# Performance work log

Measured on AMD Instinct MI355X. Metric: run time of the kernel, lower is better.

## Reference

```python
import jax, jax.numpy as jnp
import numpy as np

DIM = 256
RADIUS = 3
DIAM = 2 * RADIUS + 1          # 7
NNEIGH = DIAM * DIAM           # 49
B, H, W = 2, 64, 64
EPS_LN = 1e-6
EPS_NORM = 1e-7


def conv1x1(x, w, b):
    # x: [B,Cin,H,W], w: [Cout,Cin], b: [Cout]
    return jnp.einsum('oi,bihw->bohw', w, x) + b[None, :, None, None]


def layernorm2d(x, g, b):
    # channel-wise norm as in LayerNorm2d (mean/var over channel dim)
    u = x.mean(1, keepdims=True)
    s = ((x - u) ** 2).mean(1, keepdims=True)
    xn = (x - u) / jnp.sqrt(s + EPS_LN)
    return g[None, :, None, None] * xn + b[None, :, None, None]


def unfold_reflect(x, r):
    # torch F.unfold(pad(x, reflect, r), kernel=2r+1).reshape(B,C,D*D,H,W)
    d = 2 * r + 1
    hh, ww = x.shape[2], x.shape[3]
    xp = jnp.pad(x, ((0, 0), (0, 0), (r, r), (r, r)), mode='reflect')
    pats = [xp[:, :, i:i + hh, j:j + ww] for i in range(d) for j in range(d)]
    return jnp.stack(pats, axis=2)  # [B,C,D*D,H,W]


def setup_inputs() -> dict:
    key = jax.random.key(0)
    ks = jax.random.split(key, 20)
    sc_c = 1.0 / np.sqrt(DIM)
    sc_f = 1.0 / np.sqrt(NNEIGH + DIM)
    inp = {
        'spatial_feats': jax.random.normal(ks[0], (B, DIM, H, W), jnp.float32),
        'semantic_feats': jax.random.normal(ks[1], (B, DIM, H, W), jnp.float32),
        # range_proj: conv1x1 -> LN2d -> SiLU -> conv1x1
        'rp_w1': jax.random.normal(ks[2], (DIM, DIM), jnp.float32) * sc_c,
        'rp_b1': jnp.zeros((DIM,), jnp.float32),
        'rp_g': jnp.ones((DIM,), jnp.float32),
        'rp_be': jnp.zeros((DIM,), jnp.float32),
        'rp_w2': jax.random.normal(ks[3], (DIM, DIM), jnp.float32) * sc_c,
        'rp_b2': jnp.zeros((DIM,), jnp.float32),
        # fixup_proj: conv1x1(49+C->49) -> LN2d -> SiLU -> conv1x1(49->49)
        'fp_w1': jax.random.normal(ks[4], (NNEIGH, NNEIGH + DIM), jnp.float32) * sc_f,
        'fp_b1': jnp.zeros((NNEIGH,), jnp.float32),
        'fp_g': jnp.ones((NNEIGH,), jnp.float32),
        'fp_be': jnp.zeros((NNEIGH,), jnp.float32),
        'fp_w2': jax.random.normal(ks[5], (NNEIGH, NNEIGH), jnp.float32) * (1.0 / np.sqrt(NNEIGH)),
        'fp_b2': jnp.zeros((NNEIGH,), jnp.float32),
        # output_proj: conv1x1 -> LN2d -> conv1x1
        'op_w1': jax.random.normal(ks[6], (DIM, DIM), jnp.float32) * sc_c,
        'op_b1': jnp.zeros((DIM,), jnp.float32),
        'op_g': jnp.ones((DIM,), jnp.float32),
        'op_be': jnp.zeros((DIM,), jnp.float32),
        'op_w2': jax.random.normal(ks[7], (DIM, DIM), jnp.float32) * sc_c,
        'op_b2': jnp.zeros((DIM,), jnp.float32),
        'sigma_spatial': jnp.ones((), jnp.float32),
    }
    return inp


def reference(spatial_feats, semantic_feats,
              rp_w1, rp_b1, rp_g, rp_be, rp_w2, rp_b2,
              fp_w1, fp_b1, fp_g, fp_be, fp_w2, fp_b2,
              op_w1, op_b1, op_g, op_be, op_w2, op_b2,
              sigma_spatial):
    scale = jnp.asarray(DIM ** 0.5, spatial_feats.dtype)
    # range_proj(semantic_feats)
    px = conv1x1(semantic_feats, rp_w1, rp_b1)
    px = jax.nn.silu(layernorm2d(px, rp_g, rp_be))
    px = conv1x1(px, rp_w2, rp_b2)  # [B,C,H,W]

    # spatial (Gaussian) kernel over the window
    lin = jnp.linspace(-1.0, 1.0, DIAM)
    xg, yg = jnp.meshgrid(lin, lin, indexing='ij')
    spatial_kernel = jnp.exp(-(xg ** 2 + yg ** 2) / (2.0 * sigma_spatial ** 2))
    spatial_kernel = spatial_kernel.reshape(1, NNEIGH, 1, 1)

    # range kernel: local similarity + softmax over the 49 neighbors
    queries = unfold_reflect(px, RADIUS)                       # [B,C,N,H,W]
    sim = jnp.einsum('bcnhw,bchw->bnhw', queries, px) / scale
    range_kernel = jax.nn.softmax(sim.astype(jnp.float32), axis=1).astype(px.dtype)

    # neighborhoods of spatial features
    neighborhoods = unfold_reflect(spatial_feats, RADIUS)      # [B,C,N,H,W]

    # gated fixup correction
    ck = range_kernel * spatial_kernel                          # [B,N,H,W]
    fx = conv1x1(jnp.concatenate([ck, semantic_feats], axis=1), fp_w1, fp_b1)
    fx = jax.nn.silu(layernorm2d(fx, fp_g, fp_be))
    fx = conv1x1(fx, fp_w2, fp_b2)
    ck = ck + ck * jax.nn.sigmoid(fx)
    ck = ck / (ck.sum(1, keepdims=True) + EPS_NORM)

    # weighted neighborhood sum
    out = jnp.einsum('bcnhw,bnhw->bchw', neighborhoods, ck)

    # output_proj (note: no SiLU here, matching the module)
    out = conv1x1(out, op_w1, op_b1)
    out = layernorm2d(out, op_g, op_be)
    out = conv1x1(out, op_w2, op_b2)
    return out
```

## Files before the change

### kernel.cpp

```cpp
#include <hip/hip_runtime.h>
#include <cstdint>

#define HW 4096
#define C_ 256
#define NN 49
#define KW 305

typedef __bf16 bf16;
typedef bf16 bf16x8 __attribute__((ext_vector_type(8)));
typedef bf16 bf16x4 __attribute__((ext_vector_type(4)));
typedef bf16 bf16x2 __attribute__((ext_vector_type(2)));
typedef float f32x4 __attribute__((ext_vector_type(4)));

#define GLD16(src, dst) __builtin_amdgcn_global_load_lds( \
    (const __attribute__((address_space(1))) uint32_t*)(src), \
    (__attribute__((address_space(3))) uint32_t*)(dst), 16, 0, 0)

__device__ __forceinline__ int refl(int i) { return i < 0 ? -i : (i > 63 ? 126 - i : i); }
__device__ __forceinline__ float sigmoidf_(float x) { return 1.f / (1.f + __expf(-x)); }

__global__ __launch_bounds__(256) void prep_all(const float* __restrict__ rp_w1,
                                                const float* __restrict__ rp_w2,
                                                const float* __restrict__ op_w1,
                                                const float* __restrict__ op_w2,
                                                const float* __restrict__ fp_w1,
                                                const float* __restrict__ sigma,
                                                bf16* __restrict__ wrp1, bf16* __restrict__ wrp2,
                                                bf16* __restrict__ wop1, bf16* __restrict__ wop2,
                                                float* __restrict__ w1ckg, bf16* __restrict__ w1sb,
                                                float* __restrict__ sk)
{
    int bid = blockIdx.x;
    if (bid < 256) {
        const float* src = (bid < 64) ? rp_w1 : (bid < 128) ? rp_w2 : (bid < 192) ? op_w1 : op_w2;
        bf16* dst = (bid < 64) ? wrp1 : (bid < 128) ? wrp2 : (bid < 192) ? wop1 : wop2;
        int i = ((bid & 63) * 256 + threadIdx.x) * 4;
        f32x4 v = *(const f32x4*)&src[i];
        bf16x4 o = {(bf16)v[0], (bf16)v[1], (bf16)v[2], (bf16)v[3]};
        *(bf16x4*)&dst[i] = o;
    } else if (bid == 256) {
        int n = threadIdx.x;
        if (n < NN) {
            int i = n / 7, j = n % 7;
            float xg = (i - 3) * (1.f / 3.f), yg = (j - 3) * (1.f / 3.f);
            float s = sigma[0];
            sk[n] = __expf(-(xg * xg + yg * yg) / (2.f * s * s));
        }
    } else if (bid < 270) {
        int idx = (bid - 257) * 256 + threadIdx.x;
        if (idx < NN * 64) {
            int k = idx >> 6, o = idx & 63;
            w1ckg[idx] = (o < NN) ? fp_w1[o * KW + k] : 0.f;
        }
    } else {
        int idx = (bid - 270) * 256 + threadIdx.x;
        int o = idx >> 8, c = idx & 255;
        w1sb[idx] = (o < NN) ? (bf16)fp_w1[o * KW + NN + c] : (bf16)0.f;
    }
}

__global__ __launch_bounds__(256) void cvtT_k(const float* __restrict__ spatial,
                                              const float* __restrict__ semantic,
                                              bf16* __restrict__ spb, bf16* __restrict__ seb)
{
    __shared__ float tile[32][33];
    int z = blockIdx.z;
    int b = z & 1;
    const float* src = (z >> 1) ? semantic : spatial;
    bf16* dst = (z >> 1) ? seb : spb;
    int p0 = blockIdx.x * 32, c0 = blockIdx.y * 32;
    int tx = threadIdx.x & 31, ty = threadIdx.x >> 5;
    const float* s = src + (size_t)b * C_ * HW;
    #pragma unroll
    for (int i = 0; i < 32; i += 8)
        tile[ty + i][tx] = s[(size_t)(c0 + ty + i) * HW + p0 + tx];
    __syncthreads();
    int p = threadIdx.x >> 3, cq = (threadIdx.x & 7) * 4;
    bf16x4 o = {(bf16)tile[cq][p], (bf16)tile[cq + 1][p], (bf16)tile[cq + 2][p], (bf16)tile[cq + 3][p]};
    *(bf16x4*)&dst[((size_t)b * HW + p0 + p) * C_ + c0 + cq] = o;
}

__device__ __forceinline__ void stage_b(const bf16* __restrict__ Wp, bf16* dst, int kc, int t)
{
    const bf16* gB = Wp + (size_t)(t >> 2) * C_ + kc + (((t & 3) ^ ((t >> 3) & 3)) * 8);
    #pragma unroll
    for (int ii = 0; ii < 4; ++ii)
        GLD16(gB + (size_t)ii * 64 * C_, dst + ii * 2048 + t * 8);
}

template<bool SILU, int MODE>
__global__ __launch_bounds__(256) void conv_pair(const bf16* __restrict__ X,
                                                 const bf16* __restrict__ W1,
                                                 const float* __restrict__ b1v,
                                                 const float* __restrict__ g,
                                                 const float* __restrict__ be,
                                                 const bf16* __restrict__ W2,
                                                 const float* __restrict__ b2v,
                                                 void* __restrict__ Yv)
{
    __shared__ bf16 Xf[16 * 256];
    __shared__ bf16 Mid[16 * 256];
    __shared__ bf16 Bs[2][256 * 32];
    __shared__ float lnred[16][4][2];
    const int t = threadIdx.x;
    const int lane = t & 63, wc = t >> 6;
    const int l15 = lane & 15, kb = lane >> 4;
    const long q0 = (long)blockIdx.x * 16;

    {
        const int row = t >> 5, slot = t & 31;
        const bf16* gX = X + (q0 + row) * C_ + (slot ^ (row & 7)) * 8;
        GLD16(gX, &Xf[t * 8]);
        GLD16(gX + 8 * C_, &Xf[2048 + t * 8]);
    }
    stage_b(W1, &Bs[0][0], 0, t);

    const int ax7 = l15 & 7;
    const int bsl = (kb ^ ((l15 >> 1) & 3)) * 8;
    int boff[4];
    #pragma unroll
    for (int n = 0; n < 4; ++n)
        boff[n] = (wc * 64 + n * 16 + l15) * 32 + bsl;

    f32x4 acc[4];
    #pragma unroll
    for (int n = 0; n < 4; ++n) acc[n] = (f32x4){0.f, 0.f, 0.f, 0.f};

    __syncthreads();
    int cur = 0;
    #pragma unroll
    for (int ks = 0; ks < 8; ++ks) {
        if (ks < 7) stage_b(W1, &Bs[cur ^ 1][0], (ks + 1) * 32, t);
        bf16x8 a = *(const bf16x8*)&Xf[l15 * 256 + ((ks * 4 + kb) ^ ax7) * 8];
        #pragma unroll
        for (int n = 0; n < 4; ++n) {
            bf16x8 b = *(const bf16x8*)&Bs[cur][boff[n]];
            acc[n] = __builtin_amdgcn_mfma_f32_16x16x32_bf16(a, b, acc[n], 0, 0, 0);
        }
        __syncthreads();
        cur ^= 1;
    }

    stage_b(W2, &Bs[0][0], 0, t);

    float s4[4] = {0.f, 0.f, 0.f, 0.f}, ss4[4] = {0.f, 0.f, 0.f, 0.f};
    #pragma unroll
    for (int n = 0; n < 4; ++n) {
        float bo = b1v[wc * 64 + n * 16 + l15];
        #pragma unroll
        for (int r = 0; r < 4; ++r) {
            float v = acc[n][r] + bo;
            acc[n][r] = v;
            s4[r] += v; ss4[r] += v * v;
        }
    }
    #pragma unroll
    for (int off = 1; off <= 8; off <<= 1) {
        #pragma unroll
        for (int r = 0; r < 4; ++r) {
            s4[r]  += __shfl_xor(s4[r], off, 64);
            ss4[r] += __shfl_xor(ss4[r], off, 64);
        }
    }
    if (l15 == 0) {
        #pragma unroll
        for (int r = 0; r < 4; ++r) {
            lnred[kb * 4 + r][wc][0] = s4[r];
            lnred[kb * 4 + r][wc][1] = ss4[r];
        }
    }
    __syncthreads();
    float mean[4], rstd[4];
    #pragma unroll
    for (int r = 0; r < 4; ++r) {
        int p = kb * 4 + r;
        float st  = lnred[p][0][0] + lnred[p][1][0] + lnred[p][2][0] + lnred[p][3][0];
        float sst = lnred[p][0][1] + lnred[p][1][1] + lnred[p][2][1] + lnred[p][3][1];
        mean[r] = st * (1.f / 256.f);
        float var = sst * (1.f / 256.f) - mean[r] * mean[r];
        rstd[r] = rsqrtf(var + 1e-6f);
    }
    #pragma unroll
    for (int n = 0; n < 4; ++n) {
        int ch = wc * 64 + n * 16 + l15;
        float gv = g[ch], bev = be[ch];
        #pragma unroll
        for (int r = 0; r < 4; ++r) {
            float y = (acc[n][r] - mean[r]) * rstd[r] * gv + bev;
            if (SILU) y *= sigmoidf_(y);
            int p = kb * 4 + r;
            Mid[p * 256 + (((ch >> 3) ^ (p & 7)) * 8) + (ch & 7)] = (bf16)y;
        }
    }
    __syncthreads();

    f32x4 acc2[4];
    #pragma unroll
    for (int n = 0; n < 4; ++n) acc2[n] = (f32x4){0.f, 0.f, 0.f, 0.f};
    cur = 0;
    #pragma unroll
    for (int ks = 0; ks < 8; ++ks) {
        if (ks < 7) stage_b(W2, &Bs[cur ^ 1][0], (ks + 1) * 32, t);
        bf16x8 a = *(const bf16x8*)&Mid[l15 * 256 + ((ks * 4 + kb) ^ ax7) * 8];
        #pragma unroll
        for (int n = 0; n < 4; ++n) {
            bf16x8 b = *(const bf16x8*)&Bs[cur][boff[n]];
            acc2[n] = __builtin_amdgcn_mfma_f32_16x16x32_bf16(a, b, acc2[n], 0, 0, 0);
        }
        __syncthreads();
        cur ^= 1;
    }

    if constexpr (MODE == 0) {
        #pragma unroll
        for (int n = 0; n < 4; ++n) {
            int ch = wc * 64 + n * 16 + l15;
            float bo = b2v[ch];
            #pragma unroll
            for (int r = 0; r < 4; ++r)
                Xf[(kb * 4 + r) * 256 + ch] = (bf16)(acc2[n][r] + bo);
        }
        __syncthreads();
        bf16* Y = (bf16*)Yv;
        const int p = t >> 4, cb = (t & 15) * 16;
        bf16x8 v0 = *(const bf16x8*)&Xf[p * 256 + cb];
        bf16x8 v1 = *(const bf16x8*)&Xf[p * 256 + cb + 8];
        *(bf16x8*)&Y[(q0 + p) * C_ + cb] = v0;
        *(bf16x8*)&Y[(q0 + p) * C_ + cb + 8] = v1;
    } else {
        float* Y = (float*)Yv;
        const int bb = (int)(q0 >> 12);
        const int pp = (int)(q0 & 4095) + kb * 4;
        #pragma unroll
        for (int n = 0; n < 4; ++n) {
            int ch = wc * 64 + n * 16 + l15;
            float bo = b2v[ch];
            f32x4 val = {acc2[n][0] + bo, acc2[n][1] + bo, acc2[n][2] + bo, acc2[n][3] + bo};
            *(f32x4*)&Y[((size_t)bb * C_ + ch) * HW + pp] = val;
        }
    }
}

__global__ __launch_bounds__(256) void attn_k(const bf16* __restrict__ px,
                                              const bf16* __restrict__ spb,
                                              const bf16* __restrict__ seb,
                                              const bf16* __restrict__ w1sb,
                                              const float* __restrict__ w1ckg,
                                              const float* __restrict__ b1,
                                              const float* __restrict__ w2,
                                              const float* __restrict__ b2,
                                              const float* __restrict__ g,
                                              const float* __restrict__ be,
                                              const float* __restrict__ sk,
                                              bf16* __restrict__ outb)
{
    __shared__ float S[112 * 17];
    __shared__ float fxs[64 * 17];
    __shared__ float w1ck[NN * 64];
    __shared__ float w2l[NN][51];
    __shared__ float ckl[16][64];
    __shared__ float hb[4][64];
    __shared__ bf16 spatl[128 * 128];

    const int t = threadIdx.x, lane = t & 63, wid = t >> 6;
    const int l15 = lane & 15, kb = lane >> 4;
    const int blk = blockIdx.x;
    const int batch = blk >> 8, tt = blk & 255;
    const int h0 = (tt >> 4) * 4, w0 = (tt & 15) * 4;
    const long base = (long)batch * HW;

    #pragma unroll
    for (int i = 0; i < 13; ++i) {
        int idx = i * 256 + t;
        if (idx < NN * 64) w1ck[idx] = w1ckg[idx];
    }
    for (int idx = t; idx < NN * NN; idx += 256)
        w2l[idx / NN][idx % NN] = w2[idx];

    const int ppy = l15 >> 2, ppx = l15 & 3;
    const long qB = base + (h0 + ppy) * 64 + (w0 + ppx);
    const bf16* bpxp = px + qB * C_ + kb * 8;
    const bf16* bsemp = seb + qB * C_ + kb * 8;

    bool valid[3], ispx[3];
    const bf16* arow[3];
    #pragma unroll
    for (int j = 0; j < 3; ++j) {
        int tid = wid + 4 * j;
        valid[j] = tid < 11;
        ispx[j] = tid < 7;
        int u = tid * 16 + l15;
        int uy = (u * 205) >> 11, ux = u - uy * 10;
        long grow = (u < 100) ? base + refl(h0 + uy - 3) * 64 + refl(w0 + ux - 3) : base;
        int o = (tid - 7) * 16 + l15;
        arow[j] = ispx[j] ? (px + grow * C_ + kb * 8)
                          : (w1sb + (size_t)(o & 63) * C_ + kb * 8);
    }

    f32x4 acc[3];
    #pragma unroll
    for (int j = 0; j < 3; ++j) acc[j] = (f32x4){0.f, 0.f, 0.f, 0.f};

    #pragma unroll
    for (int ks = 0; ks < 8; ++ks) {
        bf16x8 bp = *(const bf16x8*)(bpxp + ks * 32);
        bf16x8 bs = *(const bf16x8*)(bsemp + ks * 32);
        #pragma unroll
        for (int j = 0; j < 3; ++j) {
            if (valid[j]) {
                bf16x8 a = *(const bf16x8*)(arow[j] + ks * 32);
                acc[j] = __builtin_amdgcn_mfma_f32_16x16x32_bf16(a, ispx[j] ? bp : bs, acc[j], 0, 0, 0);
            }
        }
    }
    #pragma unroll
    for (int j = 0; j < 3; ++j) {
        if (valid[j]) {
            int tid = wid + 4 * j;
            float* dst = ispx[j] ? &S[(tid * 16 + kb * 4) * 17 + l15]
                                 : &fxs[((tid - 7) * 16 + kb * 4) * 17 + l15];
            dst[0] = acc[j][0]; dst[17] = acc[j][1]; dst[34] = acc[j][2]; dst[51] = acc[j][3];
        }
    }

    const bf16* growp[8];
    {
        const int us = t >> 4, ss = t & 15;
        #pragma unroll
        for (int i = 0; i < 8; ++i) {
            int uu = i * 16 + us;
            int uy = (uu * 205) >> 11, ux = uu - uy * 10;
            long grow = (uu < 100) ? base + refl(h0 + uy - 3) * 64 + refl(w0 + ux - 3) : base;
            growp[i] = spb + grow * C_ + ss * 8;
            GLD16(growp[i], &spatl[uu * 128 + ss * 8]);
        }
    }
    __syncthreads();

    const float skv = (lane < NN) ? sk[lane] : 0.f;
    const int nn_ = (lane < NN) ? lane : 0;
    const int dy = nn_ / 7, dx = nn_ % 7;
    #pragma unroll
    for (int j = 0; j < 4; ++j) {
        int p = wid * 4 + j, py = p >> 2, px4 = p & 3;
        int u = (py + dy) * 10 + px4 + dx;
        float sval = (lane < NN) ? S[u * 17 + p] * 0.0625f : -1e30f;
        float mx = sval;
        #pragma unroll
        for (int off = 32; off; off >>= 1) mx = fmaxf(mx, __shfl_xor(mx, off, 64));
        float ev = (lane < NN) ? __expf(sval - mx) : 0.f;
        float ssum = ev;
        #pragma unroll
        for (int off = 32; off; off >>= 1) ssum += __shfl_xor(ssum, off, 64);
        ckl[p][lane] = (lane < NN) ? (ev / ssum) * skv : 0.f;
    }

    const float bo  = (lane < NN) ? b1[lane] : 0.f;
    const float gl  = (lane < NN) ? g[lane] : 0.f;
    const float bel = (lane < NN) ? be[lane] : 0.f;
    const float b2l = (lane < NN) ? b2[lane] : 0.f;
    #pragma unroll
    for (int j = 0; j < 4; ++j) {
        int p = wid * 4 + j;
        float fx = fxs[lane * 17 + p] + bo;
        #pragma unroll 7
        for (int k = 0; k < NN; ++k) fx += w1ck[k * 64 + lane] * ckl[p][k];
        float s = fx, ss = fx * fx;
        #pragma unroll
        for (int off = 32; off; off >>= 1) {
            s  += __shfl_xor(s, off, 64);
            ss += __shfl_xor(ss, off, 64);
        }
        float mean = s * (1.f / 49.f);
        float var  = ss * (1.f / 49.f) - mean * mean;
        float rstd = rsqrtf(var + 1e-6f);
        float hv = 0.f;
        if (lane < NN) {
            float xn = (fx - mean) * rstd * gl + bel;
            hv = xn * sigmoidf_(xn);
        }
        hb[wid][lane] = hv;
        float ckv = 0.f;
        if (lane < NN) {
            float fx2 = b2l;
            #pragma unroll 7
            for (int k = 0; k < NN; ++k) fx2 += w2l[lane][k] * hb[wid][k];
            ckv = ckl[p][lane] * (1.f + sigmoidf_(fx2));
        }
        float tot = ckv;
        #pragma unroll
        for (int off = 32; off; off >>= 1) tot += __shfl_xor(tot, off, 64);
        ckl[p][lane] = (lane < NN) ? ckv / (tot + 1e-7f) : 0.f;
    }

    #pragma unroll
    for (int ci = 0; ci < 2; ++ci) {
        if (ci == 1) {
            __syncthreads();
            const int ss = t & 15;
            #pragma unroll
            for (int i = 0; i < 8; ++i) {
                int uu = i * 16 + (t >> 4);
                GLD16(growp[i] + 128, &spatl[uu * 128 + ss * 8]);
            }
            __syncthreads();
        }
        #pragma unroll
        for (int j = 0; j < 4; ++j) {
            int p = wid * 4 + j, py = p >> 2, px4 = p & 3;
            long q = base + (h0 + py) * 64 + (w0 + px4);
            int ub = py * 10 + px4;
            float a0 = 0.f, a1 = 0.f;
            #pragma unroll
            for (int n = 0; n < NN; ++n) {
                int u = ub + (n / 7) * 10 + (n % 7);
                float cv = ckl[p][n];
                bf16x2 v = *(const bf16x2*)&spatl[u * 128 + lane * 2];
                a0 += cv * (float)v[0];
                a1 += cv * (float)v[1];
            }
            bf16x2 ov = {(bf16)a0, (bf16)a1};
            *(bf16x2*)&outb[q * C_ + ci * 128 + lane * 2] = ov;
        }
    }
}

extern "C" void kernel_launch(void* const* d_in, const int* in_sizes, int n_in,
                              void* d_out, int out_size, void* d_ws, size_t ws_size,
                              hipStream_t stream)
{
    const float* spatial  = (const float*)d_in[0];
    const float* semantic = (const float*)d_in[1];
    const float* rp_w1 = (const float*)d_in[2];
    const float* rp_b1 = (const float*)d_in[3];
    const float* rp_g  = (const float*)d_in[4];
    const float* rp_be = (const float*)d_in[5];
    const float* rp_w2 = (const float*)d_in[6];
    const float* rp_b2 = (const float*)d_in[7];
    const float* fp_w1 = (const float*)d_in[8];
    const float* fp_b1 = (const float*)d_in[9];
    const float* fp_g  = (const float*)d_in[10];
    const float* fp_be = (const float*)d_in[11];
    const float* fp_w2 = (const float*)d_in[12];
    const float* fp_b2 = (const float*)d_in[13];
    const float* op_w1 = (const float*)d_in[14];
    const float* op_b1 = (const float*)d_in[15];
    const float* op_g  = (const float*)d_in[16];
    const float* op_be = (const float*)d_in[17];
    const float* op_w2 = (const float*)d_in[18];
    const float* op_b2 = (const float*)d_in[19];
    const float* sigma = (const float*)d_in[20];

    const size_t NPX = 2 * (size_t)HW;
    float* ws = (float*)d_ws;
    float* sk    = ws;
    float* w1ckg = sk + 64;
    bf16* bfbase = (bf16*)(w1ckg + 3200);
    bf16* spb = bfbase;
    bf16* seb = spb + NPX * C_;
    bf16* t0  = seb + NPX * C_;
    bf16* t1  = t0  + NPX * C_;
    bf16* wrp1 = t1 + NPX * C_;
    bf16* wrp2 = wrp1 + C_ * C_;
    bf16* wop1 = wrp2 + C_ * C_;
    bf16* wop2 = wop1 + C_ * C_;
    bf16* w1sb = wop2 + C_ * C_;

    prep_all<<<334, 256, 0, stream>>>(rp_w1, rp_w2, op_w1, op_w2, fp_w1, sigma,
                                      wrp1, wrp2, wop1, wop2, w1ckg, w1sb, sk);
    cvtT_k<<<dim3(128, 8, 4), 256, 0, stream>>>(spatial, semantic, spb, seb);

    conv_pair<true, 0><<<512, 256, 0, stream>>>(seb, wrp1, rp_b1, rp_g, rp_be, wrp2, rp_b2, t1);

    attn_k<<<512, 256, 0, stream>>>(t1, spb, seb, w1sb, w1ckg, fp_b1, fp_w2, fp_b2,
                                    fp_g, fp_be, sk, t0);

    conv_pair<false, 1><<<512, 256, 0, stream>>>(t0, wop1, op_b1, op_g, op_be, wop2, op_b2, d_out);
}
```

Baseline: 75.54 us.

## Merge prep kernels, double conv row tile, restructure attention staging

Fuses the weight-prep and transpose kernels into one setup launch, and doubles the conv_pair tile to 32 pixels so each staged weight tile feeds two MFMA row groups, halving the grid. The attention kernel now stages the full 256-channel spatial neighborhood once into a swizzled shared buffer, where the old code made two 128-channel passes. The similarity MFMAs reuse that shared buffer, the fixup weights are held in registers or stored as bf16 transposed, and the weighted sum uses 8-wide vector loads. This trims launch overhead, global reloads and barriers, but conv_pair runs fewer blocks and attention needs more registers and shared memory, which can lower occupancy.

```diff
diff --git a/kernel.cpp b/kernel.cpp
--- a/kernel.cpp
+++ b/kernel.cpp
@@ -19,65 +19,72 @@
 __device__ __forceinline__ int refl(int i) { return i < 0 ? -i : (i > 63 ? 126 - i : i); }
 __device__ __forceinline__ float sigmoidf_(float x) { return 1.f / (1.f + __expf(-x)); }
 
-__global__ __launch_bounds__(256) void prep_all(const float* __restrict__ rp_w1,
-                                                const float* __restrict__ rp_w2,
-                                                const float* __restrict__ op_w1,
-                                                const float* __restrict__ op_w2,
-                                                const float* __restrict__ fp_w1,
-                                                const float* __restrict__ sigma,
-                                                bf16* __restrict__ wrp1, bf16* __restrict__ wrp2,
-                                                bf16* __restrict__ wop1, bf16* __restrict__ wop2,
-                                                float* __restrict__ w1ckg, bf16* __restrict__ w1sb,
-                                                float* __restrict__ sk)
+__global__ __launch_bounds__(256) void setup_k(const float* __restrict__ spatial,
+                                               const float* __restrict__ semantic,
+                                               const float* __restrict__ rp_w1,
+                                               const float* __restrict__ rp_w2,
+                                               const float* __restrict__ op_w1,
+                                               const float* __restrict__ op_w2,
+                                               const float* __restrict__ fp_w1,
+                                               const float* __restrict__ fp_w2,
+                                               const float* __restrict__ sigma,
+                                               bf16* __restrict__ spb, bf16* __restrict__ seb,
+                                               bf16* __restrict__ wrp1, bf16* __restrict__ wrp2,
+                                               bf16* __restrict__ wop1, bf16* __restrict__ wop2,
+                                               float* __restrict__ w1ckg, bf16* __restrict__ w1sb,
+                                               bf16* __restrict__ w2Tg, float* __restrict__ sk)
 {
-    int bid = blockIdx.x;
-    if (bid < 256) {
-        const float* src = (bid < 64) ? rp_w1 : (bid < 128) ? rp_w2 : (bid < 192) ? op_w1 : op_w2;
-        bf16* dst = (bid < 64) ? wrp1 : (bid < 128) ? wrp2 : (bid < 192) ? wop1 : wop2;
-        int i = ((bid & 63) * 256 + threadIdx.x) * 4;
+    __shared__ float tile[32][33];
+    const int bid = blockIdx.x, t = threadIdx.x;
+    if (bid < 4096) {
+        int z = bid >> 10, r = bid & 1023;
+        int b = z & 1;
+        const float* src = (z >> 1) ? semantic : spatial;
+        bf16* dst = (z >> 1) ? seb : spb;
+        int p0 = (r & 127) * 32, c0 = (r >> 7) * 32;
+        int tx = t & 31, ty = t >> 5;
+        const float* s = src + (size_t)b * C_ * HW;
+        #pragma unroll
+        for (int i = 0; i < 32; i += 8)
+            tile[ty + i][tx] = s[(size_t)(c0 + ty + i) * HW + p0 + tx];
+        __syncthreads();
+        int p = t >> 3, cq = (t & 7) * 4;
+        bf16x4 o = {(bf16)tile[cq][p], (bf16)tile[cq + 1][p], (bf16)tile[cq + 2][p], (bf16)tile[cq + 3][p]};
+        *(bf16x4*)&dst[((size_t)b * HW + p0 + p) * C_ + c0 + cq] = o;
+        return;
+    }
+    int pid = bid - 4096;
+    if (pid < 256) {
+        const float* src = (pid < 64) ? rp_w1 : (pid < 128) ? rp_w2 : (pid < 192) ? op_w1 : op_w2;
+        bf16* dst = (pid < 64) ? wrp1 : (pid < 128) ? wrp2 : (pid < 192) ? wop1 : wop2;
+        int i = ((pid & 63) * 256 + t) * 4;
         f32x4 v = *(const f32x4*)&src[i];
         bf16x4 o = {(bf16)v[0], (bf16)v[1], (bf16)v[2], (bf16)v[3]};
         *(bf16x4*)&dst[i] = o;
-    } else if (bid == 256) {
-        int n = threadIdx.x;
-        if (n < NN) {
-            int i = n / 7, j = n % 7;
+    } else if (pid == 256) {
+        if (t < NN) {
+            int i = t / 7, j = t % 7;
             float xg = (i - 3) * (1.f / 3.f), yg = (j - 3) * (1.f / 3.f);
             float s = sigma[0];
-            sk[n] = __expf(-(xg * xg + yg * yg) / (2.f * s * s));
-        }
-    } else if (bid < 270) {
-        int idx = (bid - 257) * 256 + threadIdx.x;
+            sk[t] = __expf(-(xg * xg + yg * yg) / (2.f * s * s));
+        }
+    } else if (pid < 270) {
+        int idx = (pid - 257) * 256 + t;
         if (idx < NN * 64) {
             int k = idx >> 6, o = idx & 63;
             w1ckg[idx] = (o < NN) ? fp_w1[o * KW + k] : 0.f;
         }
-    } else {
-        int idx = (bid - 270) * 256 + threadIdx.x;
+    } else if (pid < 334) {
+        int idx = (pid - 270) * 256 + t;
         int o = idx >> 8, c = idx & 255;
         w1sb[idx] = (o < NN) ? (bf16)fp_w1[o * KW + NN + c] : (bf16)0.f;
-    }
-}
-
-__global__ __launch_bounds__(256) void cvtT_k(const float* __restrict__ spatial,
-                                              const float* __restrict__ semantic,
-                                              bf16* __restrict__ spb, bf16* __restrict__ seb)
-{
-    __shared__ float tile[32][33];
-    int z = blockIdx.z;
-    int b = z & 1;
-    const float* src = (z >> 1) ? semantic : spatial;
-    bf16* dst = (z >> 1) ? seb : spb;
-    int p0 = blockIdx.x * 32, c0 = blockIdx.y * 32;
-    int tx = threadIdx.x & 31, ty = threadIdx.x >> 5;
-    const float* s = src + (size_t)b * C_ * HW;
-    #pragma unroll
-    for (int i = 0; i < 32; i += 8)
-        tile[ty + i][tx] = s[(size_t)(c0 + ty + i) * HW + p0 + tx];
-    __syncthreads();
-    int p = threadIdx.x >> 3, cq = (threadIdx.x & 7) * 4;
-    bf16x4 o = {(bf16)tile[cq][p], (bf16)tile[cq + 1][p], (bf16)tile[cq + 2][p], (bf16)tile[cq + 3][p]};
-    *(bf16x4*)&dst[((size_t)b * HW + p0 + p) * C_ + c0 + cq] = o;
+    } else {
+        int idx = (pid - 334) * 256 + t;
+        if (idx < NN * 64) {
+            int k = idx >> 6, o = idx & 63;
+            w2Tg[idx] = (o < NN) ? (bf16)fp_w2[o * NN + k] : (bf16)0.f;
+        }
+    }
 }
 
 __device__ __forceinline__ void stage_b(const bf16* __restrict__ Wp, bf16* dst, int kc, int t)
@@ -98,44 +105,52 @@
                                                  const float* __restrict__ b2v,
                                                  void* __restrict__ Yv)
 {
-    __shared__ bf16 Xf[16 * 256];
-    __shared__ bf16 Mid[16 * 256];
-    __shared__ bf16 Bs[2][256 * 32];
-    __shared__ float lnred[16][4][2];
+    __shared__ __align__(16) bf16 Xf[32 * 256];
+    __shared__ __align__(16) bf16 Mid[32 * 256];
+    __shared__ __align__(16) bf16 Bs[2][256 * 32];
+    __shared__ float lnred[32][4][2];
     const int t = threadIdx.x;
     const int lane = t & 63, wc = t >> 6;
     const int l15 = lane & 15, kb = lane >> 4;
-    const long q0 = (long)blockIdx.x * 16;
+    const long q0 = (long)blockIdx.x * 32;
 
     {
-        const int row = t >> 5, slot = t & 31;
-        const bf16* gX = X + (q0 + row) * C_ + (slot ^ (row & 7)) * 8;
-        GLD16(gX, &Xf[t * 8]);
-        GLD16(gX + 8 * C_, &Xf[2048 + t * 8]);
+        const int r8 = t >> 5, slot = t & 31;
+        const bf16* gX = X + (q0 + r8) * C_ + ((slot ^ (r8 & 7)) * 8);
+        #pragma unroll
+        for (int i = 0; i < 4; ++i)
+            GLD16(gX + (size_t)i * 8 * C_, &Xf[i * 2048 + t * 8]);
     }
     stage_b(W1, &Bs[0][0], 0, t);
 
-    const int ax7 = l15 & 7;
+    const int x7 = l15 & 7;
     const int bsl = (kb ^ ((l15 >> 1) & 3)) * 8;
     int boff[4];
     #pragma unroll
     for (int n = 0; n < 4; ++n)
         boff[n] = (wc * 64 + n * 16 + l15) * 32 + bsl;
-
-    f32x4 acc[4];
-    #pragma unroll
-    for (int n = 0; n < 4; ++n) acc[n] = (f32x4){0.f, 0.f, 0.f, 0.f};
+    const int a0base = l15 * 256;
+    const int a1base = (16 + l15) * 256;
+
+    f32x4 acc[2][4];
+    #pragma unroll
+    for (int m = 0; m < 2; ++m)
+        #pragma unroll
+        for (int n = 0; n < 4; ++n) acc[m][n] = (f32x4){0.f, 0.f, 0.f, 0.f};
 
     __syncthreads();
     int cur = 0;
     #pragma unroll
     for (int ks = 0; ks < 8; ++ks) {
         if (ks < 7) stage_b(W1, &Bs[cur ^ 1][0], (ks + 1) * 32, t);
-        bf16x8 a = *(const bf16x8*)&Xf[l15 * 256 + ((ks * 4 + kb) ^ ax7) * 8];
+        const int ko = ((ks * 4 + kb) ^ x7) * 8;
+        bf16x8 a0 = *(const bf16x8*)&Xf[a0base + ko];
+        bf16x8 a1 = *(const bf16x8*)&Xf[a1base + ko];
         #pragma unroll
         for (int n = 0; n < 4; ++n) {
             bf16x8 b = *(const bf16x8*)&Bs[cur][boff[n]];
-            acc[n] = __builtin_amdgcn_mfma_f32_16x16x32_bf16(a, b, acc[n], 0, 0, 0);
+            acc[0][n] = __builtin_amdgcn_mfma_f32_16x16x32_bf16(a0, b, acc[0][n], 0, 0, 0);
+            acc[1][n] = __builtin_amdgcn_mfma_f32_16x16x32_bf16(a1, b, acc[1][n], 0, 0, 0);
         }
         __syncthreads();
         cur ^= 1;
@@ -143,69 +158,87 @@
 
     stage_b(W2, &Bs[0][0], 0, t);
 
-    float s4[4] = {0.f, 0.f, 0.f, 0.f}, ss4[4] = {0.f, 0.f, 0.f, 0.f};
+    float s4[2][4], ss4[2][4];
+    #pragma unroll
+    for (int m = 0; m < 2; ++m)
+        #pragma unroll
+        for (int r = 0; r < 4; ++r) { s4[m][r] = 0.f; ss4[m][r] = 0.f; }
     #pragma unroll
     for (int n = 0; n < 4; ++n) {
         float bo = b1v[wc * 64 + n * 16 + l15];
         #pragma unroll
+        for (int m = 0; m < 2; ++m)
+            #pragma unroll
+            for (int r = 0; r < 4; ++r) {
+                float v = acc[m][n][r] + bo;
+                acc[m][n][r] = v;
+                s4[m][r] += v; ss4[m][r] += v * v;
+            }
+    }
+    #pragma unroll
+    for (int off = 1; off <= 8; off <<= 1)
+        #pragma unroll
+        for (int m = 0; m < 2; ++m)
+            #pragma unroll
+            for (int r = 0; r < 4; ++r) {
+                s4[m][r]  += __shfl_xor(s4[m][r], off, 64);
+                ss4[m][r] += __shfl_xor(ss4[m][r], off, 64);
+            }
+    if (l15 == 0) {
+        #pragma unroll
+        for (int m = 0; m < 2; ++m)
+            #pragma unroll
+            for (int r = 0; r < 4; ++r) {
+                lnred[m * 16 + kb * 4 + r][wc][0] = s4[m][r];
+                lnred[m * 16 + kb * 4 + r][wc][1] = ss4[m][r];
+            }
+    }
+    __syncthreads();
+    float mean[2][4], rstd[2][4];
+    #pragma unroll
+    for (int m = 0; m < 2; ++m)
+        #pragma unroll
         for (int r = 0; r < 4; ++r) {
-            float v = acc[n][r] + bo;
-            acc[n][r] = v;
-            s4[r] += v; ss4[r] += v * v;
-        }
-    }
-    #pragma unroll
-    for (int off = 1; off <= 8; off <<= 1) {
-        #pragma unroll
-        for (int r = 0; r < 4; ++r) {
-            s4[r]  += __shfl_xor(s4[r], off, 64);
-            ss4[r] += __shfl_xor(ss4[r], off, 64);
-        }
-    }
-    if (l15 == 0) {
-        #pragma unroll
-        for (int r = 0; r < 4; ++r) {
-            lnred[kb * 4 + r][wc][0] = s4[r];
-            lnred[kb * 4 + r][wc][1] = ss4[r];
-        }
-    }
-    __syncthreads();
-    float mean[4], rstd[4];
-    #pragma unroll
-    for (int r = 0; r < 4; ++r) {
-        int p = kb * 4 + r;
-        float st  = lnred[p][0][0] + lnred[p][1][0] + lnred[p][2][0] + lnred[p][3][0];
-        float sst = lnred[p][0][1] + lnred[p][1][1] + lnred[p][2][1] + lnred[p][3][1];
-        mean[r] = st * (1.f / 256.f);
-        float var = sst * (1.f / 256.f) - mean[r] * mean[r];
-        rstd[r] = rsqrtf(var + 1e-6f);
-    }
+            int p = m * 16 + kb * 4 + r;
+            float st  = lnred[p][0][0] + lnred[p][1][0] + lnred[p][2][0] + lnred[p][3][0];
+            float sst = lnred[p][0][1] + lnred[p][1][1] + lnred[p][2][1] + lnred[p][3][1];
+            mean[m][r] = st * (1.f / 256.f);
+            float var = sst * (1.f / 256.f) - mean[m][r] * mean[m][r];
+            rstd[m][r] = rsqrtf(var + 1e-6f);
+        }
     #pragma unroll
     for (int n = 0; n < 4; ++n) {
         int ch = wc * 64 + n * 16 + l15;
         float gv = g[ch], bev = be[ch];
         #pragma unroll
-        for (int r = 0; r < 4; ++r) {
-            float y = (acc[n][r] - mean[r]) * rstd[r] * gv + bev;
-            if (SILU) y *= sigmoidf_(y);
-            int p = kb * 4 + r;
-            Mid[p * 256 + (((ch >> 3) ^ (p & 7)) * 8) + (ch & 7)] = (bf16)y;
-        }
+        for (int m = 0; m < 2; ++m)
+            #pragma unroll
+            for (int r = 0; r < 4; ++r) {
+                float y = (acc[m][n][r] - mean[m][r]) * rstd[m][r] * gv + bev;
+                if (SILU) y *= sigmoidf_(y);
+                int p = m * 16 + kb * 4 + r;
+                Mid[p * 256 + (((ch >> 3) ^ (p & 7)) * 8) + (ch & 7)] = (bf16)y;
+            }
     }
     __syncthreads();
 
-    f32x4 acc2[4];
-    #pragma unroll
-    for (int n = 0; n < 4; ++n) acc2[n] = (f32x4){0.f, 0.f, 0.f, 0.f};
+    f32x4 acc2[2][4];
+    #pragma unroll
+    for (int m = 0; m < 2; ++m)
+        #pragma unroll
+        for (int n = 0; n < 4; ++n) acc2[m][n] = (f32x4){0.f, 0.f, 0.f, 0.f};
     cur = 0;
     #pragma unroll
     for (int ks = 0; ks < 8; ++ks) {
         if (ks < 7) stage_b(W2, &Bs[cur ^ 1][0], (ks + 1) * 32, t);
-        bf16x8 a = *(const bf16x8*)&Mid[l15 * 256 + ((ks * 4 + kb) ^ ax7) * 8];
+        const int ko = ((ks * 4 + kb) ^ x7) * 8;
+        bf16x8 a0 = *(const bf16x8*)&Mid[a0base + ko];
+        bf16x8 a1 = *(const bf16x8*)&Mid[a1base + ko];
         #pragma unroll
         for (int n = 0; n < 4; ++n) {
             bf16x8 b = *(const bf16x8*)&Bs[cur][boff[n]];
-            acc2[n] = __builtin_amdgcn_mfma_f32_16x16x32_bf16(a, b, acc2[n], 0, 0, 0);
+            acc2[0][n] = __builtin_amdgcn_mfma_f32_16x16x32_bf16(a0, b, acc2[0][n], 0, 0, 0);
+            acc2[1][n] = __builtin_amdgcn_mfma_f32_16x16x32_bf16(a1, b, acc2[1][n], 0, 0, 0);
         }
         __syncthreads();
         cur ^= 1;
@@ -217,26 +250,33 @@
             int ch = wc * 64 + n * 16 + l15;
             float bo = b2v[ch];
             #pragma unroll
-            for (int r = 0; r < 4; ++r)
-                Xf[(kb * 4 + r) * 256 + ch] = (bf16)(acc2[n][r] + bo);
+            for (int m = 0; m < 2; ++m)
+                #pragma unroll
+                for (int r = 0; r < 4; ++r)
+                    Xf[(m * 16 + kb * 4 + r) * 256 + ch] = (bf16)(acc2[m][n][r] + bo);
         }
         __syncthreads();
         bf16* Y = (bf16*)Yv;
-        const int p = t >> 4, cb = (t & 15) * 16;
-        bf16x8 v0 = *(const bf16x8*)&Xf[p * 256 + cb];
-        bf16x8 v1 = *(const bf16x8*)&Xf[p * 256 + cb + 8];
-        *(bf16x8*)&Y[(q0 + p) * C_ + cb] = v0;
-        *(bf16x8*)&Y[(q0 + p) * C_ + cb + 8] = v1;
+        const int p = t >> 3, cb = (t & 7) * 32;
+        #pragma unroll
+        for (int i = 0; i < 4; ++i) {
+            bf16x8 v = *(const bf16x8*)&Xf[p * 256 + cb + i * 8];
+            *(bf16x8*)&Y[(q0 + p) * C_ + cb + i * 8] = v;
+        }
     } else {
         float* Y = (float*)Yv;
         const int bb = (int)(q0 >> 12);
-        const int pp = (int)(q0 & 4095) + kb * 4;
         #pragma unroll
         for (int n = 0; n < 4; ++n) {
             int ch = wc * 64 + n * 16 + l15;
             float bo = b2v[ch];
-            f32x4 val = {acc2[n][0] + bo, acc2[n][1] + bo, acc2[n][2] + bo, acc2[n][3] + bo};
-            *(f32x4*)&Y[((size_t)bb * C_ + ch) * HW + pp] = val;
+            #pragma unroll
+            for (int m = 0; m < 2; ++m) {
+                int pp = (int)(q0 & 4095) + m * 16 + kb * 4;
+                f32x4 val = {acc2[m][n][0] + bo, acc2[m][n][1] + bo,
+                             acc2[m][n][2] + bo, acc2[m][n][3] + bo};
+                *(f32x4*)&Y[((size_t)bb * C_ + ch) * HW + pp] = val;
+            }
         }
     }
 }
@@ -246,21 +286,20 @@
                                               const bf16* __restrict__ seb,
                                               const bf16* __restrict__ w1sb,
                                               const float* __restrict__ w1ckg,
+                                              const bf16* __restrict__ w2Tg,
                                               const float* __restrict__ b1,
-                                              const float* __restrict__ w2,
                                               const float* __restrict__ b2,
                                               const float* __restrict__ g,
                                               const float* __restrict__ be,
                                               const float* __restrict__ sk,
                                               bf16* __restrict__ outb)
 {
+    __shared__ __align__(16) bf16 uni[112 * 256];
     __shared__ float S[112 * 17];
     __shared__ float fxs[64 * 17];
-    __shared__ float w1ck[NN * 64];
-    __shared__ float w2l[NN][51];
+    __shared__ __align__(16) bf16 w2lT[NN * 64];
     __shared__ float ckl[16][64];
     __shared__ float hb[4][64];
-    __shared__ bf16 spatl[128 * 128];
 
     const int t = threadIdx.x, lane = t & 63, wid = t >> 6;
     const int l15 = lane & 15, kb = lane >> 4;
@@ -269,73 +308,87 @@
     const int h0 = (tt >> 4) * 4, w0 = (tt & 15) * 4;
     const long base = (long)batch * HW;
 
+    {
+        #pragma unroll
+        for (int i = 0; i < 13; ++i) {
+            int st = i * 256 + t;
+            if (st < 3200) {
+                int u = st >> 5, s = st & 31;
+                int uy = (u * 205) >> 11, ux = u - uy * 10;
+                long grow = base + refl(h0 + uy - 3) * 64 + refl(w0 + ux - 3);
+                GLD16(px + grow * C_ + ((s ^ (u & 7)) * 8), &uni[u * 256 + s * 8]);
+            }
+        }
+        GLD16(w2Tg + t * 8, &w2lT[t * 8]);
+        if (t < 136) GLD16(w2Tg + (256 + t) * 8, &w2lT[(256 + t) * 8]);
+    }
+
+    const int ppy = l15 >> 2, ppx = l15 & 3;
+    const int u_p = 33 + ppy * 10 + ppx;
+    const int bpbase = u_p * 256, bx7 = u_p & 7;
+    const long qB = base + (h0 + ppy) * 64 + (w0 + ppx);
+    const bf16* bsemp = seb + qB * C_ + kb * 8;
+    const int x7 = l15 & 7;
+
+    const int tid0 = wid, tid1 = wid + 4, tid2 = wid + 8;
+    const bool t1sim = (tid1 < 7);
+    const bool t2valid = (tid2 < 11);
+    const int a0base = (tid0 * 16 + l15) * 256;
+    const int a1base = (tid1 * 16 + l15) * 256;
+    const bf16* a1g = w1sb + (size_t)(((tid1 - 7) & 3) * 16 + l15) * C_ + kb * 8;
+    const bf16* a2g = w1sb + (size_t)(((tid2 - 7) & 3) * 16 + l15) * C_ + kb * 8;
+
+    f32x4 acc0 = {0.f, 0.f, 0.f, 0.f}, acc1 = {0.f, 0.f, 0.f, 0.f}, acc2 = {0.f, 0.f, 0.f, 0.f};
+
+    __syncthreads();
+
+    #pragma unroll
+    for (int ks = 0; ks < 8; ++ks) {
+        const int kg = ks * 4 + kb;
+        bf16x8 bp = *(const bf16x8*)&uni[bpbase + ((kg ^ bx7) * 8)];
+        bf16x8 a0 = *(const bf16x8*)&uni[a0base + ((kg ^ x7) * 8)];
+        acc0 = __builtin_amdgcn_mfma_f32_16x16x32_bf16(a0, bp, acc0, 0, 0, 0);
+        bf16x8 bs = *(const bf16x8*)(bsemp + ks * 32);
+        bf16x8 a1;
+        if (t1sim) a1 = *(const bf16x8*)&uni[a1base + ((kg ^ x7) * 8)];
+        else       a1 = *(const bf16x8*)(a1g + ks * 32);
+        acc1 = __builtin_amdgcn_mfma_f32_16x16x32_bf16(a1, t1sim ? bp : bs, acc1, 0, 0, 0);
+        if (t2valid) {
+            bf16x8 a2 = *(const bf16x8*)(a2g + ks * 32);
+            acc2 = __builtin_amdgcn_mfma_f32_16x16x32_bf16(a2, bs, acc2, 0, 0, 0);
+        }
+    }
+    {
+        float* dst = &S[(tid0 * 16 + kb * 4) * 17 + l15];
+        dst[0] = acc0[0]; dst[17] = acc0[1]; dst[34] = acc0[2]; dst[51] = acc0[3];
+    }
+    if (t1sim) {
+        float* dst = &S[(tid1 * 16 + kb * 4) * 17 + l15];
+        dst[0] = acc1[0]; dst[17] = acc1[1]; dst[34] = acc1[2]; dst[51] = acc1[3];
+    } else {
+        float* dst = &fxs[(kb * 4) * 17 + l15];
+        dst[0] = acc1[0]; dst[17] = acc1[1]; dst[34] = acc1[2]; dst[51] = acc1[3];
+    }
+    if (t2valid) {
+        float* dst = &fxs[((tid2 - 7) * 16 + kb * 4) * 17 + l15];
+        dst[0] = acc2[0]; dst[17] = acc2[1]; dst[34] = acc2[2]; dst[51] = acc2[3];
+    }
+    __syncthreads();
+
     #pragma unroll
     for (int i = 0; i < 13; ++i) {
-        int idx = i * 256 + t;
-        if (idx < NN * 64) w1ck[idx] = w1ckg[idx];
-    }
-    for (int idx = t; idx < NN * NN; idx += 256)
-        w2l[idx / NN][idx % NN] = w2[idx];
-
-    const int ppy = l15 >> 2, ppx = l15 & 3;
-    const long qB = base + (h0 + ppy) * 64 + (w0 + ppx);
-    const bf16* bpxp = px + qB * C_ + kb * 8;
-    const bf16* bsemp = seb + qB * C_ + kb * 8;
-
-    bool valid[3], ispx[3];
-    const bf16* arow[3];
-    #pragma unroll
-    for (int j = 0; j < 3; ++j) {
-        int tid = wid + 4 * j;
-        valid[j] = tid < 11;
-        ispx[j] = tid < 7;
-        int u = tid * 16 + l15;
-        int uy = (u * 205) >> 11, ux = u - uy * 10;
-        long grow = (u < 100) ? base + refl(h0 + uy - 3) * 64 + refl(w0 + ux - 3) : base;
-        int o = (tid - 7) * 16 + l15;
-        arow[j] = ispx[j] ? (px + grow * C_ + kb * 8)
-                          : (w1sb + (size_t)(o & 63) * C_ + kb * 8);
-    }
-
-    f32x4 acc[3];
-    #pragma unroll
-    for (int j = 0; j < 3; ++j) acc[j] = (f32x4){0.f, 0.f, 0.f, 0.f};
-
-    #pragma unroll
-    for (int ks = 0; ks < 8; ++ks) {
-        bf16x8 bp = *(const bf16x8*)(bpxp + ks * 32);
-        bf16x8 bs = *(const bf16x8*)(bsemp + ks * 32);
-        #pragma unroll
-        for (int j = 0; j < 3; ++j) {
-            if (valid[j]) {
-                bf16x8 a = *(const bf16x8*)(arow[j] + ks * 32);
-                acc[j] = __builtin_amdgcn_mfma_f32_16x16x32_bf16(a, ispx[j] ? bp : bs, acc[j], 0, 0, 0);
-            }
-        }
-    }
-    #pragma unroll
-    for (int j = 0; j < 3; ++j) {
-        if (valid[j]) {
-            int tid = wid + 4 * j;
-            float* dst = ispx[j] ? &S[(tid * 16 + kb * 4) * 17 + l15]
-                                 : &fxs[((tid - 7) * 16 + kb * 4) * 17 + l15];
-            dst[0] = acc[j][0]; dst[17] = acc[j][1]; dst[34] = acc[j][2]; dst[51] = acc[j][3];
-        }
-    }
-
-    const bf16* growp[8];
-    {
-        const int us = t >> 4, ss = t & 15;
-        #pragma unroll
-        for (int i = 0; i < 8; ++i) {
-            int uu = i * 16 + us;
-            int uy = (uu * 205) >> 11, ux = uu - uy * 10;
-            long grow = (uu < 100) ? base + refl(h0 + uy - 3) * 64 + refl(w0 + ux - 3) : base;
-            growp[i] = spb + grow * C_ + ss * 8;
-            GLD16(growp[i], &spatl[uu * 128 + ss * 8]);
-        }
-    }
-    __syncthreads();
+        int st = i * 256 + t;
+        if (st < 3200) {
+            int u = st >> 5, s = st & 31;
+            int uy = (u * 205) >> 11, ux = u - uy * 10;
+            long grow = base + refl(h0 + uy - 3) * 64 + refl(w0 + ux - 3);
+            GLD16(spb + grow * C_ + ((s ^ (u & 7)) * 8), &uni[u * 256 + s * 8]);
+        }
+    }
+
+    float w1r[NN];
+    #pragma unroll
+    for (int k = 0; k < NN; ++k) w1r[k] = w1ckg[k * 64 + lane];
 
     const float skv = (lane < NN) ? sk[lane] : 0.f;
     const int nn_ = (lane < NN) ? lane : 0;
@@ -364,7 +417,7 @@
         int p = wid * 4 + j;
         float fx = fxs[lane * 17 + p] + bo;
         #pragma unroll 7
-        for (int k = 0; k < NN; ++k) fx += w1ck[k * 64 + lane] * ckl[p][k];
+        for (int k = 0; k < NN; ++k) fx += w1r[k] * ckl[p][k];
         float s = fx, ss = fx * fx;
         #pragma unroll
         for (int off = 32; off; off >>= 1) {
@@ -384,7 +437,7 @@
         if (lane < NN) {
             float fx2 = b2l;
             #pragma unroll 7
-            for (int k = 0; k < NN; ++k) fx2 += w2l[lane][k] * hb[wid][k];
+            for (int k = 0; k < NN; ++k) fx2 += (float)w2lT[k * 64 + lane] * hb[wid][k];
             ckv = ckl[p][lane] * (1.f + sigmoidf_(fx2));
         }
         float tot = ckv;
@@ -392,36 +445,32 @@
         for (int off = 32; off; off >>= 1) tot += __shfl_xor(tot, off, 64);
         ckl[p][lane] = (lane < NN) ? ckv / (tot + 1e-7f) : 0.f;
     }
-
-    #pragma unroll
-    for (int ci = 0; ci < 2; ++ci) {
-        if (ci == 1) {
-            __syncthreads();
-            const int ss = t & 15;
-            #pragma unroll
-            for (int i = 0; i < 8; ++i) {
-                int uu = i * 16 + (t >> 4);
-                GLD16(growp[i] + 128, &spatl[uu * 128 + ss * 8]);
-            }
-            __syncthreads();
-        }
-        #pragma unroll
-        for (int j = 0; j < 4; ++j) {
-            int p = wid * 4 + j, py = p >> 2, px4 = p & 3;
-            long q = base + (h0 + py) * 64 + (w0 + px4);
-            int ub = py * 10 + px4;
-            float a0 = 0.f, a1 = 0.f;
-            #pragma unroll
-            for (int n = 0; n < NN; ++n) {
-                int u = ub + (n / 7) * 10 + (n % 7);
-                float cv = ckl[p][n];
-                bf16x2 v = *(const bf16x2*)&spatl[u * 128 + lane * 2];
-                a0 += cv * (float)v[0];
-                a1 += cv * (float)v[1];
-            }
-            bf16x2 ov = {(bf16)a0, (bf16)a1};
-            *(bf16x2*)&outb[q * C_ + ci * 128 + lane * 2] = ov;
-        }
+    __syncthreads();
+
+    const int hh_ = lane >> 5, l31 = lane & 31;
+    #pragma unroll
+    for (int jj = 0; jj < 2; ++jj) {
+        int p = wid * 4 + jj * 2 + hh_;
+        int py = p >> 2, px4 = p & 3;
+        long q = base + (h0 + py) * 64 + (w0 + px4);
+        int ub = py * 10 + px4;
+        float a[8];
+        #pragma unroll
+        for (int e = 0; e < 8; ++e) a[e] = 0.f;
+        for (int dyy = 0; dyy < 7; ++dyy) {
+            #pragma unroll
+            for (int dxx = 0; dxx < 7; ++dxx) {
+                int u = ub + dyy * 10 + dxx;
+                float cv = ckl[p][dyy * 7 + dxx];
+                bf16x8 v = *(const bf16x8*)&uni[u * 256 + ((l31 ^ (u & 7)) * 8)];
+                #pragma unroll
+                for (int e = 0; e < 8; ++e) a[e] += cv * (float)v[e];
+            }
+        }
+        bf16x8 ov;
+        #pragma unroll
+        for (int e = 0; e < 8; ++e) ov[e] = (bf16)a[e];
+        *(bf16x8*)&outb[q * C_ + l31 * 8] = ov;
     }
 }
 
@@ -465,15 +514,17 @@
     bf16* wop1 = wrp2 + C_ * C_;
     bf16* wop2 = wop1 + C_ * C_;
     bf16* w1sb = wop2 + C_ * C_;
-
-    prep_all<<<334, 256, 0, stream>>>(rp_w1, rp_w2, op_w1, op_w2, fp_w1, sigma,
-                                      wrp1, wrp2, wop1, wop2, w1ckg, w1sb, sk);
-    cvtT_k<<<dim3(128, 8, 4), 256, 0, stream>>>(spatial, semantic, spb, seb);
-
-    conv_pair<true, 0><<<512, 256, 0, stream>>>(seb, wrp1, rp_b1, rp_g, rp_be, wrp2, rp_b2, t1);
-
-    attn_k<<<512, 256, 0, stream>>>(t1, spb, seb, w1sb, w1ckg, fp_b1, fp_w2, fp_b2,
+    bf16* w2Tg = w1sb + 64 * C_;
+
+    setup_k<<<4443, 256, 0, stream>>>(spatial, semantic, rp_w1, rp_w2, op_w1, op_w2,
+                                      fp_w1, fp_w2, sigma,
+                                      spb, seb, wrp1, wrp2, wop1, wop2,
+                                      w1ckg, w1sb, w2Tg, sk);
+
+    conv_pair<true, 0><<<256, 256, 0, stream>>>(seb, wrp1, rp_b1, rp_g, rp_be, wrp2, rp_b2, t1);
+
+    attn_k<<<512, 256, 0, stream>>>(t1, spb, seb, w1sb, w1ckg, w2Tg, fp_b1, fp_b2,
                                     fp_g, fp_be, sk, t0);
 
-    conv_pair<false, 1><<<512, 256, 0, stream>>>(t0, wop1, op_b1, op_g, op_be, wop2, op_b2, d_out);
+    conv_pair<false, 1><<<256, 256, 0, stream>>>(t0, wop1, op_b1, op_g, op_be, wop2, op_b2, d_out);
 }
```

New measurement: 73.45 us. 2.8% less time.
